# Kernel tuning notes

Measured on AMD Instinct MI355X. Metric: run time of the kernel, lower is better.

Reference implementation:

```python
import jax, jax.numpy as jnp
import numpy as np
from jax import lax

NEG_SLOPE = 0.1

def leaky(x):
    return jnp.where(x >= 0, x, NEG_SLOPE * x)

def soft_pool(x, n_p):
    # x: (B, F, P) -> (B, F, N_p, F), faithful to the torch per-channel topk+gather
    xs = jax.nn.softmax(x, axis=1)
    _, idx = lax.top_k(xs, n_p)                 # idx: (B, F, N_p), indices into P per channel
    # sp_cube[b, c, n, f] = xs[b, c, idx[b, f, n]]
    g = jnp.take_along_axis(xs[:, :, None, :], idx[:, None, :, :], axis=3)  # (B, F, F, N_p)
    return jnp.transpose(g, (0, 1, 3, 2))       # (B, F, N_p, F)

def setup_inputs() -> dict:
    key = jax.random.key(0)
    ks = jax.random.split(key, 16)
    B, C, H, W, M = 32, 5, 64, 64, 8
    s = 0.02
    inp = {
        'coor_feat': jax.random.uniform(ks[0], (B, C, H, W), jnp.float32),
        'region': jax.random.uniform(ks[1], (B, M, H, W), jnp.float32),
        'extents': jax.random.uniform(ks[2], (B, 3), jnp.float32),
        'w1': jax.random.normal(ks[3], (128, C), jnp.float32) * s,
        'b1': jnp.zeros((128,), jnp.float32),
        'w2': jax.random.normal(ks[4], (128, 128), jnp.float32) * s,
        'b2': jnp.zeros((128,), jnp.float32),
        'w3': jax.random.normal(ks[5], (128, 128), jnp.float32) * s,
        'b3': jnp.zeros((128,), jnp.float32),
        'w_sp': jax.random.normal(ks[6], (128, 128, 128), jnp.float32) * s,  # (out, in, k) for Conv2d(128,128,(1,128))
        'b_sp': jnp.zeros((128,), jnp.float32),
        'fc1_w': jax.random.normal(ks[7], (512, 128 * 8), jnp.float32) * s,
        'fc1_b': jnp.zeros((512,), jnp.float32),
        'fc2_w': jax.random.normal(ks[8], (256, 512), jnp.float32) * s,
        'fc2_b': jnp.zeros((256,), jnp.float32),
        'fcr_w': jax.random.normal(ks[9], (4, 256), jnp.float32) * 0.01,
        'fcr_b': jnp.zeros((4,), jnp.float32),
        'fct_w': jax.random.normal(ks[10], (3, 256), jnp.float32) * 0.01,
        'fct_b': jnp.zeros((3,), jnp.float32),
    }
    return inp

def reference(coor_feat, region, extents, w1, b1, w2, b2, w3, b3, w_sp, b_sp,
              fc1_w, fc1_b, fc2_w, fc2_b, fcr_w, fcr_b, fct_w, fct_b):
    bs, in_c, fh, fw = coor_feat.shape
    num_regions = region.shape[1]
    # denormalize xyz channels by extents (in_c == 5 path)
    xyz = (coor_feat[:, :3] - 0.5) * extents[:, :, None, None]
    x = jnp.concatenate([xyz, coor_feat[:, 3:]], axis=1)
    x = x.reshape(bs, in_c, fh * fw)                          # (B, C, P)
    # 1x1 Conv1d stack
    x = leaky(jnp.einsum('bip,oi->bop', x, w1) + b1[None, :, None])
    x = leaky(jnp.einsum('bip,oi->bop', x, w2) + b2[None, :, None])
    x = jnp.einsum('bip,oi->bop', x, w3) + b3[None, :, None]  # (B, 128, P)
    # region-masked multiply: (B,128,M,P)
    xm = x[:, :, None, :] * region.reshape(bs, 1, num_regions, fh * fw)
    # spatial max pool over P
    x = jnp.max(xm, axis=-1)                                  # (B, 128, M)
    # region softpool
    sp = soft_pool(x, num_regions)                            # (B, 128, M(=N_p), 128)
    x = leaky(jnp.einsum('bcrk,ock->bor', sp, w_sp) + b_sp[None, :, None])  # conv_sp
    x = x.reshape(bs, -1)                                     # (B, 1024)
    x = leaky(x @ fc1_w.T + fc1_b)
    x = leaky(x @ fc2_w.T + fc2_b)
    rot = x @ fcr_w.T + fcr_b
    t = x @ fct_w.T + fct_b
    return (rot, t)
```

## Files before the change

kernel.cpp:

```cpp
#include <hip/hip_runtime.h>
#include <cstddef>
#include <cstdint>

#define LEAKY(s) ((s) >= 0.f ? (s) : 0.1f * (s))

constexpr int PTS    = 4096;
constexpr int NBATCH = 32;
constexpr int NM     = 8;
constexpr int TILE   = 128;
constexpr int NTILES = PTS / TILE;

constexpr size_t OFF_POOL = 0;
constexpr size_t OFF_WSP  = 131072;
constexpr size_t OFF_Y32  = 262144;
constexpr size_t OFF_Y    = 4456448;
constexpr size_t OFF_H1   = 4587520;

using bf16x8 = __attribute__((ext_vector_type(8))) short;
using f32x4v = __attribute__((ext_vector_type(4))) float;
using u16x4  = __attribute__((ext_vector_type(4))) unsigned short;
using u16x8  = __attribute__((ext_vector_type(8))) unsigned short;

__device__ __forceinline__ unsigned short rbf(float x) {
  unsigned u = __float_as_uint(x);
  return (unsigned short)((u + 0x7FFFu + ((u >> 16) & 1u)) >> 16);
}

__device__ __forceinline__ unsigned encf(float f) {
  unsigned u = __float_as_uint(f);
  return (u & 0x80000000u) ? ~u : (u | 0x80000000u);
}
__device__ __forceinline__ float decf(unsigned e) {
  unsigned u = (e & 0x80000000u) ? (e ^ 0x80000000u) : ~e;
  return __uint_as_float(u);
}

__device__ __forceinline__ int swzb(int pt, int kByte) {
  return pt * 256 + (kByte ^ ((pt & 7) << 4));
}

__global__ __launch_bounds__(256) void kW(const float* __restrict__ w2,
                                          const float* __restrict__ w3,
                                          unsigned short* __restrict__ wsp,
                                          unsigned* __restrict__ pool) {
  int id = blockIdx.x * 256 + threadIdx.x;
  pool[id] = 0u;
  int layer = id >> 14, e16 = id & 16383;
  int e = e16 & 7, l15 = (e16 >> 3) & 15, l4 = (e16 >> 7) & 3,
      kt = (e16 >> 9) & 3, mt = e16 >> 11;
  int c = mt * 16 + l15, k = kt * 32 + l4 * 8 + e;
  float v = (layer ? w3 : w2)[c * 128 + k];
  wsp[layer * 16384 + e16] = rbf(v);
}

__device__ __forceinline__ void mfmaLayer8s(const unsigned short* __restrict__ W,
                                            const float* __restrict__ bias,
                                            const char* Xc,
                                            int lane, int mt, f32x4v acc[8]) {
  const int l15 = lane & 15, l4 = lane >> 4;
  {
    float4 bv = *(const float4*)(bias + mt * 16 + l4 * 4);
    f32x4v b4; b4[0] = bv.x; b4[1] = bv.y; b4[2] = bv.z; b4[3] = bv.w;
#pragma unroll
    for (int nt = 0; nt < 8; nt++) acc[nt] = b4;
  }
#pragma unroll
  for (int kt = 0; kt < 4; kt++) {
    int woff = (((mt * 4 + kt) * 4 + l4) * 16 + l15) * 8;
    bf16x8 ah = *(const bf16x8*)(W + woff);
    const int kb = (kt * 32 + l4 * 8) * 2;
#pragma unroll
    for (int nt = 0; nt < 8; nt++) {
      bf16x8 bh = *(const bf16x8*)(Xc + swzb(nt * 16 + l15, kb));
      acc[nt] = __builtin_amdgcn_mfma_f32_16x16x32_bf16(ah, bh, acc[nt], 0, 0, 0);
    }
  }
}

__global__ __launch_bounds__(512, 8) void kA(
    const float* __restrict__ coor, const float* __restrict__ region,
    const float* __restrict__ extents,
    const float* __restrict__ w1, const float* __restrict__ b1,
    const float* __restrict__ b2, const float* __restrict__ b3,
    const unsigned short* __restrict__ wsp,
    unsigned* __restrict__ pool) {
  __shared__ unsigned short X[128 * 128];
  __shared__ float reg_s[NM * TILE];
  const int tid = threadIdx.x;
  const int b = blockIdx.y;
  const int t0 = blockIdx.x * TILE;
  const int lane = tid & 63;
  const int wv = tid >> 6;
  char* Xc = (char*)X;

  {
    int m = tid >> 6, j = tid & 63;
    float2 v = *(const float2*)(region + ((size_t)b * NM + m) * PTS + t0 + j * 2);
    *(float2*)(reg_s + m * TILE + j * 2) = v;
  }
  {
    const int pt = tid & 127;
    const int chq = (tid >> 7) * 32;
    float e0 = extents[b * 3], e1 = extents[b * 3 + 1], e2 = extents[b * 3 + 2];
    float in5[5];
#pragma unroll
    for (int i = 0; i < 5; i++) in5[i] = coor[((size_t)b * 5 + i) * PTS + t0 + pt];
    in5[0] = (in5[0] - 0.5f) * e0;
    in5[1] = (in5[1] - 0.5f) * e1;
    in5[2] = (in5[2] - 0.5f) * e2;
#pragma unroll
    for (int c8 = 0; c8 < 32; c8 += 8) {
      u16x8 hh;
#pragma unroll
      for (int q = 0; q < 8; q++) {
        int c = chq + c8 + q;
        float s = b1[c];
#pragma unroll
        for (int i = 0; i < 5; i++) s = fmaf(w1[c * 5 + i], in5[i], s);
        s = LEAKY(s);
        hh[q] = rbf(s);
      }
      int off = swzb(pt, (chq + c8) * 2);
      *(u16x8*)(Xc + off) = hh;
    }
  }
  __syncthreads();

  f32x4v acc[8];
  const int mt = wv;
  const int l15 = lane & 15, l4 = lane >> 4;

  mfmaLayer8s(wsp, b2, Xc, lane, mt, acc);
  __syncthreads();
  {
    const int ch0 = mt * 16 + l4 * 4;
#pragma unroll
    for (int nt = 0; nt < 8; nt++) {
      u16x4 h4;
#pragma unroll
      for (int r = 0; r < 4; r++) {
        float s = acc[nt][r];
        s = LEAKY(s);
        h4[r] = rbf(s);
      }
      int off = swzb(nt * 16 + l15, ch0 * 2);
      *(u16x4*)(Xc + off) = h4;
    }
  }
  __syncthreads();
  mfmaLayer8s(wsp + 16384, b3, Xc, lane, mt, acc);
  __syncthreads();

  {
    float* funnel = (float*)X;
#pragma unroll
    for (int m = 0; m < NM; m++) {
      float rv[8];
#pragma unroll
      for (int nt = 0; nt < 8; nt++) rv[nt] = reg_s[m * TILE + nt * 16 + l15];
#pragma unroll
      for (int r = 0; r < 4; r++) {
        float mx = acc[0][r] * rv[0];
#pragma unroll
        for (int nt = 1; nt < 8; nt++) mx = fmaxf(mx, acc[nt][r] * rv[nt]);
        mx = fmaxf(mx, __shfl_xor(mx, 1));
        mx = fmaxf(mx, __shfl_xor(mx, 2));
        mx = fmaxf(mx, __shfl_xor(mx, 4));
        mx = fmaxf(mx, __shfl_xor(mx, 8));
        if (l15 == 0) funnel[(mt * 16 + l4 * 4 + r) * 8 + m] = mx;
      }
    }
  }
  __syncthreads();
  {
    const float* fun = (const float*)X;
    unsigned* pl = pool + (size_t)b * 1024;
    atomicMax(pl + tid, encf(fun[tid]));
    atomicMax(pl + tid + 512, encf(fun[tid + 512]));
  }
}

__global__ __launch_bounds__(256) void kC(const unsigned* __restrict__ pool,
                                          const float* __restrict__ w_sp,
                                          float* __restrict__ y32) {
  __shared__ float As[16 * 516];
  __shared__ float xsl[4 * 128 * 8];
  __shared__ int idxL[4][4][8];
  const int tid = threadIdx.x;
  const int k0 = blockIdx.x * 4;
  const int bbase = blockIdx.y * 4;
  const int rg = tid & 63, cgq = tid >> 6;

#pragma unroll
  for (int it = 0; it < 4; it++) {
    uint4 v = *(const uint4*)(pool + (size_t)(bbase + it) * 1024 + tid * 4);
    float4 f = {decf(v.x), decf(v.y), decf(v.z), decf(v.w)};
    *(float4*)(xsl + it * 1024 + tid * 4) = f;
  }
  float4 wreg[8];
#pragma unroll
  for (int it = 0; it < 8; it++) {
    int q = tid + it * 256, o = q >> 4, cc = q & 15;
    wreg[it] = *(const float4*)(w_sp + (size_t)o * 16384 + (size_t)cc * 128 + k0);
  }
  __syncthreads();
  {
    int pair = tid >> 3, sub = tid & 7;
    int bl = pair >> 3, m = pair & 7;
    float* base = xsl + bl * 1024 + m;
    float v[16];
#pragma unroll
    for (int j = 0; j < 16; j++) v[j] = base[(sub + 8 * j) * 8];
    float mx = v[0];
#pragma unroll
    for (int j = 1; j < 16; j++) mx = fmaxf(mx, v[j]);
    mx = fmaxf(mx, __shfl_xor(mx, 1));
    mx = fmaxf(mx, __shfl_xor(mx, 2));
    mx = fmaxf(mx, __shfl_xor(mx, 4));
    float s = 0.f;
#pragma unroll
    for (int j = 0; j < 16; j++) { v[j] = expf(v[j] - mx); s += v[j]; }
    s += __shfl_xor(s, 1);
    s += __shfl_xor(s, 2);
    s += __shfl_xor(s, 4);
    float inv = 1.f / s;
#pragma unroll
    for (int j = 0; j < 16; j++) base[(sub + 8 * j) * 8] = v[j] * inv;
  }
  __syncthreads();
  if (tid < 16) {
    int bl = tid >> 2, kk = tid & 3;
    float vv[8];
#pragma unroll
    for (int n = 0; n < 8; n++) vv[n] = xsl[bl * 1024 + (k0 + kk) * 8 + n];
    int used = 0;
#pragma unroll
    for (int n = 0; n < 8; n++) {
      int best = 0; float bv = -1.f;
#pragma unroll
      for (int q = 0; q < 8; q++) {
        bool ok = ((used >> q) & 1) == 0;
        if (ok && vv[q] > bv) { bv = vv[q]; best = q; }
      }
      used |= 1 << best;
      idxL[bl][kk][n] = best;
    }
  }

  float acc[8][8];
#pragma unroll
  for (int i = 0; i < 8; i++)
#pragma unroll
    for (int j = 0; j < 8; j++) acc[i][j] = 0.f;

  for (int c0 = 0; c0 < 128; c0 += 16) {
    __syncthreads();
#pragma unroll
    for (int it = 0; it < 8; it++) {
      int q = tid + it * 256, o = q >> 4, cc = q & 15;
      As[cc * 516 + o]       = wreg[it].x;
      As[cc * 516 + 128 + o] = wreg[it].y;
      As[cc * 516 + 256 + o] = wreg[it].z;
      As[cc * 516 + 384 + o] = wreg[it].w;
    }
    __syncthreads();
    if (c0 + 16 < 128) {
#pragma unroll
      for (int it = 0; it < 8; it++) {
        int q = tid + it * 256, o = q >> 4, cc = q & 15;
        wreg[it] = *(const float4*)(w_sp + (size_t)o * 16384 + (size_t)(c0 + 16 + cc) * 128 + k0);
      }
    }
#pragma unroll
    for (int cc = 0; cc < 16; cc++) {
      float4 a0 = *(const float4*)(As + cc * 516 + rg * 4);
      float4 a1 = *(const float4*)(As + cc * 516 + 256 + rg * 4);
      float4 p0 = *(const float4*)(xsl + cgq * 1024 + (c0 + cc) * 8);
      float4 p1 = *(const float4*)(xsl + cgq * 1024 + (c0 + cc) * 8 + 4);
      float av[8] = {a0.x, a0.y, a0.z, a0.w, a1.x, a1.y, a1.z, a1.w};
      float bv[8] = {p0.x, p0.y, p0.z, p0.w, p1.x, p1.y, p1.z, p1.w};
#pragma unroll
      for (int i = 0; i < 8; i++)
#pragma unroll
        for (int j = 0; j < 8; j++) acc[i][j] = fmaf(av[i], bv[j], acc[i][j]);
    }
  }
  const int rgl = rg & 31;
  const int kkA = rg >> 5;
  int msA[8], msB[8];
#pragma unroll
  for (int r = 0; r < 8; r++) {
    msA[r] = idxL[cgq][kkA][r];
    msB[r] = idxL[cgq][2 + kkA][r];
  }
  float yp[4][8];
#pragma unroll
  for (int i4 = 0; i4 < 4; i4++) {
#pragma unroll
    for (int r = 0; r < 8; r++) {
      float v = 0.f;
#pragma unroll
      for (int j = 0; j < 8; j++) {
        v += (j == msA[r]) ? acc[i4][j] : 0.f;
        v += (j == msB[r]) ? acc[i4 + 4][j] : 0.f;
      }
      yp[i4][r] = v;
    }
  }
#pragma unroll
  for (int i4 = 0; i4 < 4; i4++)
#pragma unroll
    for (int r = 0; r < 8; r++) yp[i4][r] += __shfl_xor(yp[i4][r], 32);
  if (rg < 32) {
    float* dst = y32 + ((size_t)(bbase + cgq) * 32 + blockIdx.x) * 1024 + rgl * 32;
#pragma unroll
    for (int i4 = 0; i4 < 4; i4++) {
      float4 v0 = {yp[i4][0], yp[i4][1], yp[i4][2], yp[i4][3]};
      float4 v1 = {yp[i4][4], yp[i4][5], yp[i4][6], yp[i4][7]};
      *(float4*)(dst + i4 * 8) = v0;
      *(float4*)(dst + i4 * 8 + 4) = v1;
    }
  }
}

__global__ __launch_bounds__(256) void kY(const float* __restrict__ y32,
                                          const float* __restrict__ b_sp,
                                          float* __restrict__ y) {
  int fg = blockIdx.x, b = blockIdx.y, tid = threadIdx.x;
  int f = fg * 256 + tid;
  const float* base = y32 + (size_t)b * 32768 + f;
  float s = 0.f;
#pragma unroll 8
  for (int t = 0; t < 32; t++) s += base[t * 1024];
  s += b_sp[f >> 3];
  y[(size_t)b * 1024 + f] = LEAKY(s);
}

__global__ __launch_bounds__(256) void kE1(
    const float* __restrict__ y, const float* __restrict__ fc1_w,
    const float* __restrict__ fc1_b, float* __restrict__ h1) {
  int og = blockIdx.x, b = blockIdx.y, tid = threadIdx.x;
  int wid = tid >> 6, lane = tid & 63;
  const float4* yv = (const float4*)(y + (size_t)b * 1024);
  float4 u[4];
#pragma unroll
  for (int r = 0; r < 4; r++) u[r] = yv[r * 64 + lane];
#pragma unroll 4
  for (int pass = 0; pass < 16; pass++) {
    int o = og * 64 + pass * 4 + wid;
    const float4* wr = (const float4*)(fc1_w + (size_t)o * 1024);
    float sa = 0, sb = 0, sc = 0, sd = 0;
#pragma unroll
    for (int r = 0; r < 4; r++) {
      float4 wv = wr[r * 64 + lane];
      sa = fmaf(wv.x, u[r].x, sa); sb = fmaf(wv.y, u[r].y, sb);
      sc = fmaf(wv.z, u[r].z, sc); sd = fmaf(wv.w, u[r].w, sd);
    }
    float s = (sa + sb) + (sc + sd);
#pragma unroll
    for (int d = 1; d < 64; d <<= 1) s += __shfl_xor(s, d);
    if (lane == 0) {
      float t = s + fc1_b[o];
      h1[(size_t)b * 512 + o] = LEAKY(t);
    }
  }
}

__global__ __launch_bounds__(1024) void kE2(
    const float* __restrict__ h1, const float* __restrict__ fc2_w,
    const float* __restrict__ fc2_b,
    const float* __restrict__ fcr_w, const float* __restrict__ fcr_b,
    const float* __restrict__ fct_w, const float* __restrict__ fct_b,
    float* __restrict__ out) {
  __shared__ float h1l[512];
  __shared__ float h2[256];
  int b = blockIdx.x, tid = threadIdx.x;
  int w = tid >> 6, lane = tid & 63;
  if (tid < 128) {
    float4 v = ((const float4*)(h1 + (size_t)b * 512))[tid];
    ((float4*)h1l)[tid] = v;
  }
  __syncthreads();
  {
    const float4* h1v = (const float4*)h1l;
    float4 u0 = h1v[lane], u1 = h1v[64 + lane];
#pragma unroll 2
    for (int pass = 0; pass < 16; pass++) {
      int o = w * 16 + pass;
      const float4* wr = (const float4*)(fc2_w + (size_t)o * 512);
      float4 w0 = wr[lane], w1 = wr[64 + lane];
      float sa = fmaf(w0.x, u0.x, 0.f), sb = fmaf(w0.y, u0.y, 0.f);
      float sc = fmaf(w0.z, u0.z, 0.f), sd = fmaf(w0.w, u0.w, 0.f);
      sa = fmaf(w1.x, u1.x, sa); sb = fmaf(w1.y, u1.y, sb);
      sc = fmaf(w1.z, u1.z, sc); sd = fmaf(w1.w, u1.w, sd);
      float s = (sa + sb) + (sc + sd);
#pragma unroll
      for (int d = 1; d < 64; d <<= 1) s += __shfl_xor(s, d);
      if (lane == 0) {
        float t = s + fc2_b[o];
        h2[o] = LEAKY(t);
      }
    }
  }
  __syncthreads();
  if (w < 7) {
    bool isrot = w < 4;
    int o = isrot ? w : w - 4;
    const float4* wr = (const float4*)((isrot ? fcr_w : fct_w) + (size_t)o * 256);
    const float4* uv = (const float4*)h2;
    float4 wv = wr[lane];
    float4 u = uv[lane];
    float s = fmaf(wv.x, u.x, fmaf(wv.y, u.y, fmaf(wv.z, u.z, wv.w * u.w)));
#pragma unroll
    for (int d = 1; d < 64; d <<= 1) s += __shfl_xor(s, d);
    if (lane == 0) {
      float t = s + (isrot ? fcr_b[o] : fct_b[o]);
      out[isrot ? (b * 4 + o) : (128 + b * 3 + o)] = t;
    }
  }
}

extern "C" void kernel_launch(void* const* d_in, const int* in_sizes, int n_in,
                              void* d_out, int out_size, void* d_ws, size_t ws_size,
                              hipStream_t stream) {
  const float* coor    = (const float*)d_in[0];
  const float* region  = (const float*)d_in[1];
  const float* extents = (const float*)d_in[2];
  const float* w1 = (const float*)d_in[3];  const float* b1 = (const float*)d_in[4];
  const float* w2 = (const float*)d_in[5];  const float* b2 = (const float*)d_in[6];
  const float* w3 = (const float*)d_in[7];  const float* b3 = (const float*)d_in[8];
  const float* w_sp = (const float*)d_in[9];  const float* b_sp = (const float*)d_in[10];
  const float* fc1_w = (const float*)d_in[11]; const float* fc1_b = (const float*)d_in[12];
  const float* fc2_w = (const float*)d_in[13]; const float* fc2_b = (const float*)d_in[14];
  const float* fcr_w = (const float*)d_in[15]; const float* fcr_b = (const float*)d_in[16];
  const float* fct_w = (const float*)d_in[17]; const float* fct_b = (const float*)d_in[18];

  char* ws = (char*)d_ws;
  unsigned* pool = (unsigned*)(ws + OFF_POOL);
  unsigned short* wsp = (unsigned short*)(ws + OFF_WSP);
  float* y32  = (float*)(ws + OFF_Y32);
  float* y    = (float*)(ws + OFF_Y);
  float* h1   = (float*)(ws + OFF_H1);
  float* out  = (float*)d_out;

  kW<<<dim3(128), 256, 0, stream>>>(w2, w3, wsp, pool);
  kA<<<dim3(NTILES, NBATCH), 512, 0, stream>>>(coor, region, extents,
                                               w1, b1, b2, b3, wsp, pool);
  kC<<<dim3(32, 8), 256, 0, stream>>>(pool, w_sp, y32);
  kY<<<dim3(4, NBATCH), 256, 0, stream>>>(y32, b_sp, y);
  kE1<<<dim3(8, NBATCH), 256, 0, stream>>>(y, fc1_w, fc1_b, h1);
  kE2<<<dim3(NBATCH), 1024, 0, stream>>>(h1, fc2_w, fc2_b, fcr_w, fcr_b,
                                         fct_w, fct_b, out);
}
```

Before: 108.4 us.

## Split softmax/top-k into separate kernel and retile conv_sp over output channels

Moves the per-batch softmax and top-k index selection out of kC into a new kB kernel that writes softmax values and indices to workspace. The old kC recomputed these for every k-tile block. kC is now tiled by k and output-channel groups with all 32 batches per block, so each block loads its w_sp slice once instead of re-streaming the whole weight per batch group. The gather is done through shared memory in four passes. This adds one kernel launch and extra workspace traffic, and raises shared-memory use.

Result: slower. 131.1 us (+20.9%).

```diff
diff --git a/kernel.cpp b/kernel.cpp
--- a/kernel.cpp
+++ b/kernel.cpp
@@ -12,9 +12,11 @@
 
 constexpr size_t OFF_POOL = 0;
 constexpr size_t OFF_WSP  = 131072;
-constexpr size_t OFF_Y32  = 262144;
-constexpr size_t OFF_Y    = 4456448;
-constexpr size_t OFF_H1   = 4587520;
+constexpr size_t OFF_XS   = 196608;
+constexpr size_t OFF_IDX  = 327680;
+constexpr size_t OFF_Y32  = 458752;
+constexpr size_t OFF_Y    = 4653056;
+constexpr size_t OFF_H1   = 4784128;
 
 using bf16x8 = __attribute__((ext_vector_type(8))) short;
 using f32x4v = __attribute__((ext_vector_type(4))) float;
@@ -180,71 +182,97 @@
   }
 }
 
-__global__ __launch_bounds__(256) void kC(const unsigned* __restrict__ pool,
+__global__ __launch_bounds__(256) void kB(const unsigned* __restrict__ pool,
+                                          float* __restrict__ xs,
+                                          int* __restrict__ idx) {
+  __shared__ float pl[1024];
+  __shared__ float xsl[1024];
+  int b = blockIdx.x, tid = threadIdx.x;
+#pragma unroll
+  for (int q = 0; q < 4; q++) {
+    int p = tid + q * 256;
+    pl[p] = decf(pool[(size_t)b * 1024 + p]);
+  }
+  __syncthreads();
+  int m = tid >> 5, lane = tid & 31;
+  float v[4];
+#pragma unroll
+  for (int j = 0; j < 4; j++) v[j] = pl[(lane + 32 * j) * 8 + m];
+  float mx = fmaxf(fmaxf(v[0], v[1]), fmaxf(v[2], v[3]));
+#pragma unroll
+  for (int d = 1; d < 32; d <<= 1) mx = fmaxf(mx, __shfl_xor(mx, d, 32));
+  float e[4]; float s = 0.f;
+#pragma unroll
+  for (int j = 0; j < 4; j++) { e[j] = expf(v[j] - mx); s += e[j]; }
+#pragma unroll
+  for (int d = 1; d < 32; d <<= 1) s += __shfl_xor(s, d, 32);
+#pragma unroll
+  for (int j = 0; j < 4; j++) {
+    float x = e[j] / s;
+    int c = lane + 32 * j;
+    xsl[c * 8 + m] = x;
+    xs[(size_t)b * 1024 + c * 8 + m] = x;
+  }
+  __syncthreads();
+  if (tid < 128) {
+    float vv[8];
+#pragma unroll
+    for (int n = 0; n < 8; n++) vv[n] = xsl[tid * 8 + n];
+    int used = 0;
+#pragma unroll
+    for (int n = 0; n < 8; n++) {
+      int best = 0; float bvv = -1.f;
+#pragma unroll
+      for (int q = 0; q < 8; q++) {
+        bool ok = ((used >> q) & 1) == 0;
+        if (ok && vv[q] > bvv) { bvv = vv[q]; best = q; }
+      }
+      used |= 1 << best;
+      idx[(size_t)b * 1024 + tid * 8 + n] = best;
+    }
+  }
+}
+
+__global__ __launch_bounds__(256) void kC(const float* __restrict__ xs,
+                                          const int* __restrict__ idx,
                                           const float* __restrict__ w_sp,
                                           float* __restrict__ y32) {
-  __shared__ float As[16 * 516];
-  __shared__ float xsl[4 * 128 * 8];
-  __shared__ int idxL[4][4][8];
+  __shared__ float Ws[128 * 68];
+  __shared__ float Bs[16 * 256];
+  __shared__ int idxL[32][4][8];
   const int tid = threadIdx.x;
-  const int k0 = blockIdx.x * 4;
-  const int bbase = blockIdx.y * 4;
-  const int rg = tid & 63, cgq = tid >> 6;
-
+  const int kt = blockIdx.x, og = blockIdx.y;
+  const int k0 = kt * 4, o0 = og * 16;
+  const int rowq = tid >> 5;
+  const int bcol = tid & 31;
+  const int kown = rowq >> 1;
+
+#pragma unroll
+  for (int it = 0; it < 8; it++) {
+    int f = it * 256 + tid;
+    int o15 = f >> 7, c = f & 127;
+    float4 w = *(const float4*)(w_sp + (size_t)(o0 + o15) * 16384 + (size_t)c * 128 + k0);
+    float* wc = Ws + c * 68;
+    wc[o15]      = w.x;
+    wc[16 + o15] = w.y;
+    wc[32 + o15] = w.z;
+    wc[48 + o15] = w.w;
+  }
+  {
+    int g0 = tid * 4;
+#pragma unroll
+    for (int j = 0; j < 4; j++) {
+      int g = g0 + j;
+      int b = g >> 5, kk = (g >> 3) & 3, r = g & 7;
+      idxL[b][kk][r] = idx[(size_t)b * 1024 + (k0 + kk) * 8 + r];
+    }
+  }
+  float4 breg[4];
 #pragma unroll
   for (int it = 0; it < 4; it++) {
-    uint4 v = *(const uint4*)(pool + (size_t)(bbase + it) * 1024 + tid * 4);
-    float4 f = {decf(v.x), decf(v.y), decf(v.z), decf(v.w)};
-    *(float4*)(xsl + it * 1024 + tid * 4) = f;
-  }
-  float4 wreg[8];
-#pragma unroll
-  for (int it = 0; it < 8; it++) {
-    int q = tid + it * 256, o = q >> 4, cc = q & 15;
-    wreg[it] = *(const float4*)(w_sp + (size_t)o * 16384 + (size_t)cc * 128 + k0);
-  }
-  __syncthreads();
-  {
-    int pair = tid >> 3, sub = tid & 7;
-    int bl = pair >> 3, m = pair & 7;
-    float* base = xsl + bl * 1024 + m;
-    float v[16];
-#pragma unroll
-    for (int j = 0; j < 16; j++) v[j] = base[(sub + 8 * j) * 8];
-    float mx = v[0];
-#pragma unroll
-    for (int j = 1; j < 16; j++) mx = fmaxf(mx, v[j]);
-    mx = fmaxf(mx, __shfl_xor(mx, 1));
-    mx = fmaxf(mx, __shfl_xor(mx, 2));
-    mx = fmaxf(mx, __shfl_xor(mx, 4));
-    float s = 0.f;
-#pragma unroll
-    for (int j = 0; j < 16; j++) { v[j] = expf(v[j] - mx); s += v[j]; }
-    s += __shfl_xor(s, 1);
-    s += __shfl_xor(s, 2);
-    s += __shfl_xor(s, 4);
-    float inv = 1.f / s;
-#pragma unroll
-    for (int j = 0; j < 16; j++) base[(sub + 8 * j) * 8] = v[j] * inv;
-  }
-  __syncthreads();
-  if (tid < 16) {
-    int bl = tid >> 2, kk = tid & 3;
-    float vv[8];
-#pragma unroll
-    for (int n = 0; n < 8; n++) vv[n] = xsl[bl * 1024 + (k0 + kk) * 8 + n];
-    int used = 0;
-#pragma unroll
-    for (int n = 0; n < 8; n++) {
-      int best = 0; float bv = -1.f;
-#pragma unroll
-      for (int q = 0; q < 8; q++) {
-        bool ok = ((used >> q) & 1) == 0;
-        if (ok && vv[q] > bv) { bv = vv[q]; best = q; }
-      }
-      used |= 1 << best;
-      idxL[bl][kk][n] = best;
-    }
+    int f = it * 256 + tid;
+    int b = f & 31, mq = (f >> 5) & 1, cc = f >> 6;
+    breg[it] = *(const float4*)(xs + (size_t)b * 1024 + (size_t)cc * 8 + mq * 4);
   }
 
   float acc[8][8];
@@ -256,71 +284,63 @@
   for (int c0 = 0; c0 < 128; c0 += 16) {
     __syncthreads();
 #pragma unroll
-    for (int it = 0; it < 8; it++) {
-      int q = tid + it * 256, o = q >> 4, cc = q & 15;
-      As[cc * 516 + o]       = wreg[it].x;
-      As[cc * 516 + 128 + o] = wreg[it].y;
-      As[cc * 516 + 256 + o] = wreg[it].z;
-      As[cc * 516 + 384 + o] = wreg[it].w;
+    for (int it = 0; it < 4; it++) {
+      int f = it * 256 + tid;
+      int b = f & 31, mq = (f >> 5) & 1, cc = f >> 6;
+      *(float4*)(Bs + cc * 256 + mq * 128 + b * 4) = breg[it];
     }
     __syncthreads();
     if (c0 + 16 < 128) {
 #pragma unroll
-      for (int it = 0; it < 8; it++) {
-        int q = tid + it * 256, o = q >> 4, cc = q & 15;
-        wreg[it] = *(const float4*)(w_sp + (size_t)o * 16384 + (size_t)(c0 + 16 + cc) * 128 + k0);
+      for (int it = 0; it < 4; it++) {
+        int f = it * 256 + tid;
+        int b = f & 31, mq = (f >> 5) & 1, cc = f >> 6;
+        breg[it] = *(const float4*)(xs + (size_t)b * 1024 + (size_t)(c0 + 16 + cc) * 8 + mq * 4);
       }
     }
 #pragma unroll
     for (int cc = 0; cc < 16; cc++) {
-      float4 a0 = *(const float4*)(As + cc * 516 + rg * 4);
-      float4 a1 = *(const float4*)(As + cc * 516 + 256 + rg * 4);
-      float4 p0 = *(const float4*)(xsl + cgq * 1024 + (c0 + cc) * 8);
-      float4 p1 = *(const float4*)(xsl + cgq * 1024 + (c0 + cc) * 8 + 4);
-      float av[8] = {a0.x, a0.y, a0.z, a0.w, a1.x, a1.y, a1.z, a1.w};
-      float bv[8] = {p0.x, p0.y, p0.z, p0.w, p1.x, p1.y, p1.z, p1.w};
+      const float* wc = Ws + (c0 + cc) * 68 + rowq * 8;
+      float4 w0 = *(const float4*)(wc);
+      float4 w1 = *(const float4*)(wc + 4);
+      float4 b0 = *(const float4*)(Bs + cc * 256 + bcol * 4);
+      float4 b1 = *(const float4*)(Bs + cc * 256 + 128 + bcol * 4);
+      float av[8] = {w0.x, w0.y, w0.z, w0.w, w1.x, w1.y, w1.z, w1.w};
+      float bv[8] = {b0.x, b0.y, b0.z, b0.w, b1.x, b1.y, b1.z, b1.w};
 #pragma unroll
       for (int i = 0; i < 8; i++)
 #pragma unroll
         for (int j = 0; j < 8; j++) acc[i][j] = fmaf(av[i], bv[j], acc[i][j]);
     }
   }
-  const int rgl = rg & 31;
-  const int kkA = rg >> 5;
-  int msA[8], msB[8];
-#pragma unroll
-  for (int r = 0; r < 8; r++) {
-    msA[r] = idxL[cgq][kkA][r];
-    msB[r] = idxL[cgq][2 + kkA][r];
-  }
-  float yp[4][8];
-#pragma unroll
-  for (int i4 = 0; i4 < 4; i4++) {
-#pragma unroll
-    for (int r = 0; r < 8; r++) {
-      float v = 0.f;
-#pragma unroll
-      for (int j = 0; j < 8; j++) {
-        v += (j == msA[r]) ? acc[i4][j] : 0.f;
-        v += (j == msB[r]) ? acc[i4 + 4][j] : 0.f;
-      }
-      yp[i4][r] = v;
-    }
-  }
-#pragma unroll
-  for (int i4 = 0; i4 < 4; i4++)
-#pragma unroll
-    for (int r = 0; r < 8; r++) yp[i4][r] += __shfl_xor(yp[i4][r], 32);
-  if (rg < 32) {
-    float* dst = y32 + ((size_t)(bbase + cgq) * 32 + blockIdx.x) * 1024 + rgl * 32;
-#pragma unroll
-    for (int i4 = 0; i4 < 4; i4++) {
-      float4 v0 = {yp[i4][0], yp[i4][1], yp[i4][2], yp[i4][3]};
-      float4 v1 = {yp[i4][4], yp[i4][5], yp[i4][6], yp[i4][7]};
-      *(float4*)(dst + i4 * 8) = v0;
-      *(float4*)(dst + i4 * 8 + 4) = v1;
-    }
-  }
+  float* Dsh = Bs;
+  float yacc[16];
+#pragma unroll
+  for (int o = 0; o < 16; o++) yacc[o] = 0.f;
+  const int bown = tid >> 3, rown = tid & 7;
+#pragma unroll
+  for (int pass = 0; pass < 4; pass++) {
+    __syncthreads();
+    if (kown == pass) {
+#pragma unroll
+      for (int i = 0; i < 8; i++) {
+        int op = (rowq & 1) * 8 + i;
+        float* dp = Dsh + op * 256 + bcol * 4;
+        float4 v0 = {acc[i][0], acc[i][1], acc[i][2], acc[i][3]};
+        float4 v1 = {acc[i][4], acc[i][5], acc[i][6], acc[i][7]};
+        *(float4*)(dp) = v0;
+        *(float4*)(dp + 128) = v1;
+      }
+    }
+    __syncthreads();
+    int m = idxL[bown][pass][rown];
+    int moff = (m >> 2) * 128 + (m & 3);
+#pragma unroll
+    for (int o = 0; o < 16; o++) yacc[o] += Dsh[o * 256 + moff + bown * 4];
+  }
+  float* dst = y32 + (size_t)bown * 32768 + (size_t)kt * 1024 + (size_t)o0 * 8 + rown;
+#pragma unroll
+  for (int o = 0; o < 16; o++) dst[o * 8] = yacc[o];
 }
 
 __global__ __launch_bounds__(256) void kY(const float* __restrict__ y32,
@@ -438,6 +458,8 @@
   char* ws = (char*)d_ws;
   unsigned* pool = (unsigned*)(ws + OFF_POOL);
   unsigned short* wsp = (unsigned short*)(ws + OFF_WSP);
+  float* xs   = (float*)(ws + OFF_XS);
+  int*   idx  = (int*)(ws + OFF_IDX);
   float* y32  = (float*)(ws + OFF_Y32);
   float* y    = (float*)(ws + OFF_Y);
   float* h1   = (float*)(ws + OFF_H1);
@@ -446,7 +468,8 @@
   kW<<<dim3(128), 256, 0, stream>>>(w2, w3, wsp, pool);
   kA<<<dim3(NTILES, NBATCH), 512, 0, stream>>>(coor, region, extents,
                                                w1, b1, b2, b3, wsp, pool);
-  kC<<<dim3(32, 8), 256, 0, stream>>>(pool, w_sp, y32);
+  kB<<<dim3(NBATCH), 256, 0, stream>>>(pool, xs, idx);
+  kC<<<dim3(32, 8), 256, 0, stream>>>(xs, idx, w_sp, y32);
   kY<<<dim3(4, NBATCH), 256, 0, stream>>>(y32, b_sp, y);
   kE1<<<dim3(8, NBATCH), 256, 0, stream>>>(y, fc1_w, fc1_b, h1);
   kE2<<<dim3(NBATCH), 1024, 0, stream>>>(h1, fc2_w, fc2_b, fcr_w, fcr_b,
```

## Run first conv layer on MFMA and split kC over output-channel halves

Applied to the files above, without the earlier changes.

The first 5-to-128 pointwise layer moves from per-thread scalar FMAs to a single bf16 MFMA per tile, using a zero-padded 32-wide K layout that kW prepares for w1 and stages in a small shared buffer. The kA occupancy hint drops from 8 to 6 waves. kC now splits output channels into two halves over a 1D grid of 512 blocks with remapped indices, halving per-block registers and shared memory so more blocks run in parallel. This removes the scalar layer-1 work and kC's low parallelism, at the cost of rounding the layer-1 inputs to bf16 and an extra shuffle reduction.

New measurement: 93.26 us (median of 2 runs). -14.0%, faster.

```diff
diff --git a/kernel.cpp b/kernel.cpp
--- a/kernel.cpp
+++ b/kernel.cpp
@@ -39,18 +39,26 @@
   return pt * 256 + (kByte ^ ((pt & 7) << 4));
 }
 
-__global__ __launch_bounds__(256) void kW(const float* __restrict__ w2,
+__global__ __launch_bounds__(256) void kW(const float* __restrict__ w1,
+                                          const float* __restrict__ w2,
                                           const float* __restrict__ w3,
                                           unsigned short* __restrict__ wsp,
                                           unsigned* __restrict__ pool) {
   int id = blockIdx.x * 256 + threadIdx.x;
   pool[id] = 0u;
-  int layer = id >> 14, e16 = id & 16383;
-  int e = e16 & 7, l15 = (e16 >> 3) & 15, l4 = (e16 >> 7) & 3,
-      kt = (e16 >> 9) & 3, mt = e16 >> 11;
-  int c = mt * 16 + l15, k = kt * 32 + l4 * 8 + e;
-  float v = (layer ? w3 : w2)[c * 128 + k];
-  wsp[layer * 16384 + e16] = rbf(v);
+  {
+    int layer = id >> 14, e16 = id & 16383;
+    int e = e16 & 7, l15 = (e16 >> 3) & 15, l4 = (e16 >> 7) & 3,
+        kt = (e16 >> 9) & 3, mt = e16 >> 11;
+    int c = mt * 16 + l15, k = kt * 32 + l4 * 8 + e;
+    float v = (layer ? w3 : w2)[c * 128 + k];
+    wsp[4096 + layer * 16384 + e16] = rbf(v);
+  }
+  if (id < 4096) {
+    int e = id & 7, l15 = (id >> 3) & 15, l4 = (id >> 7) & 3, mt = id >> 9;
+    int c = mt * 16 + l15, k = l4 * 8 + e;
+    wsp[id] = (k < 5) ? rbf(w1[c * 5 + k]) : (unsigned short)0;
+  }
 }
 
 __device__ __forceinline__ void mfmaLayer8s(const unsigned short* __restrict__ W,
@@ -77,14 +85,15 @@
   }
 }
 
-__global__ __launch_bounds__(512, 8) void kA(
+__global__ __launch_bounds__(512, 6) void kA(
     const float* __restrict__ coor, const float* __restrict__ region,
     const float* __restrict__ extents,
-    const float* __restrict__ w1, const float* __restrict__ b1,
-    const float* __restrict__ b2, const float* __restrict__ b3,
+    const float* __restrict__ b1, const float* __restrict__ b2,
+    const float* __restrict__ b3,
     const unsigned short* __restrict__ wsp,
     unsigned* __restrict__ pool) {
   __shared__ unsigned short X[128 * 128];
+  __shared__ unsigned short X5[128 * 40];
   __shared__ float reg_s[NM * TILE];
   const int tid = threadIdx.x;
   const int b = blockIdx.y;
@@ -92,6 +101,7 @@
   const int lane = tid & 63;
   const int wv = tid >> 6;
   char* Xc = (char*)X;
+  char* X5c = (char*)X5;
 
   {
     int m = tid >> 6, j = tid & 63;
@@ -100,29 +110,20 @@
   }
   {
     const int pt = tid & 127;
-    const int chq = (tid >> 7) * 32;
-    float e0 = extents[b * 3], e1 = extents[b * 3 + 1], e2 = extents[b * 3 + 2];
-    float in5[5];
-#pragma unroll
-    for (int i = 0; i < 5; i++) in5[i] = coor[((size_t)b * 5 + i) * PTS + t0 + pt];
-    in5[0] = (in5[0] - 0.5f) * e0;
-    in5[1] = (in5[1] - 0.5f) * e1;
-    in5[2] = (in5[2] - 0.5f) * e2;
-#pragma unroll
-    for (int c8 = 0; c8 < 32; c8 += 8) {
-      u16x8 hh;
-#pragma unroll
-      for (int q = 0; q < 8; q++) {
-        int c = chq + c8 + q;
-        float s = b1[c];
-#pragma unroll
-        for (int i = 0; i < 5; i++) s = fmaf(w1[c * 5 + i], in5[i], s);
-        s = LEAKY(s);
-        hh[q] = rbf(s);
-      }
-      int off = swzb(pt, (chq + c8) * 2);
-      *(u16x8*)(Xc + off) = hh;
-    }
+    const int part = tid >> 7;
+    u16x8 hh = {0, 0, 0, 0, 0, 0, 0, 0};
+    if (part == 0) {
+      float e0 = extents[b * 3], e1 = extents[b * 3 + 1], e2 = extents[b * 3 + 2];
+      float in5[5];
+#pragma unroll
+      for (int i = 0; i < 5; i++) in5[i] = coor[((size_t)b * 5 + i) * PTS + t0 + pt];
+      in5[0] = (in5[0] - 0.5f) * e0;
+      in5[1] = (in5[1] - 0.5f) * e1;
+      in5[2] = (in5[2] - 0.5f) * e2;
+#pragma unroll
+      for (int q = 0; q < 5; q++) hh[q] = rbf(in5[q]);
+    }
+    *(u16x8*)(X5c + pt * 80 + part * 16) = hh;
   }
   __syncthreads();
 
@@ -130,8 +131,18 @@
   const int mt = wv;
   const int l15 = lane & 15, l4 = lane >> 4;
 
-  mfmaLayer8s(wsp, b2, Xc, lane, mt, acc);
-  __syncthreads();
+  {
+    float4 bv = *(const float4*)(b1 + mt * 16 + l4 * 4);
+    f32x4v b4; b4[0] = bv.x; b4[1] = bv.y; b4[2] = bv.z; b4[3] = bv.w;
+#pragma unroll
+    for (int nt = 0; nt < 8; nt++) acc[nt] = b4;
+    bf16x8 ah = *(const bf16x8*)(wsp + ((mt * 4 + l4) * 16 + l15) * 8);
+#pragma unroll
+    for (int nt = 0; nt < 8; nt++) {
+      bf16x8 bh = *(const bf16x8*)(X5c + (nt * 16 + l15) * 80 + l4 * 16);
+      acc[nt] = __builtin_amdgcn_mfma_f32_16x16x32_bf16(ah, bh, acc[nt], 0, 0, 0);
+    }
+  }
   {
     const int ch0 = mt * 16 + l4 * 4;
 #pragma unroll
@@ -148,7 +159,26 @@
     }
   }
   __syncthreads();
-  mfmaLayer8s(wsp + 16384, b3, Xc, lane, mt, acc);
+
+  mfmaLayer8s(wsp + 4096, b2, Xc, lane, mt, acc);
+  __syncthreads();
+  {
+    const int ch0 = mt * 16 + l4 * 4;
+#pragma unroll
+    for (int nt = 0; nt < 8; nt++) {
+      u16x4 h4;
+#pragma unroll
+      for (int r = 0; r < 4; r++) {
+        float s = acc[nt][r];
+        s = LEAKY(s);
+        h4[r] = rbf(s);
+      }
+      int off = swzb(nt * 16 + l15, ch0 * 2);
+      *(u16x4*)(Xc + off) = h4;
+    }
+  }
+  __syncthreads();
+  mfmaLayer8s(wsp + 20480, b3, Xc, lane, mt, acc);
   __syncthreads();
 
   {
@@ -183,12 +213,17 @@
 __global__ __launch_bounds__(256) void kC(const unsigned* __restrict__ pool,
                                           const float* __restrict__ w_sp,
                                           float* __restrict__ y32) {
-  __shared__ float As[16 * 516];
+  __shared__ float As[16 * 260];
   __shared__ float xsl[4 * 128 * 8];
   __shared__ int idxL[4][4][8];
   const int tid = threadIdx.x;
-  const int k0 = blockIdx.x * 4;
-  const int bbase = blockIdx.y * 4;
+  const int id = blockIdx.x;
+  const int kt = (id & 7) | ((id >> 7) << 3);
+  const int bg = (id >> 3) & 7;
+  const int og2 = (id >> 6) & 1;
+  const int k0 = kt * 4;
+  const int o0 = og2 * 64;
+  const int bbase = bg * 4;
   const int rg = tid & 63, cgq = tid >> 6;
 
 #pragma unroll
@@ -197,11 +232,11 @@
     float4 f = {decf(v.x), decf(v.y), decf(v.z), decf(v.w)};
     *(float4*)(xsl + it * 1024 + tid * 4) = f;
   }
-  float4 wreg[8];
-#pragma unroll
-  for (int it = 0; it < 8; it++) {
+  float4 wreg[4];
+#pragma unroll
+  for (int it = 0; it < 4; it++) {
     int q = tid + it * 256, o = q >> 4, cc = q & 15;
-    wreg[it] = *(const float4*)(w_sp + (size_t)o * 16384 + (size_t)cc * 128 + k0);
+    wreg[it] = *(const float4*)(w_sp + (size_t)(o0 + o) * 16384 + (size_t)cc * 128 + k0);
   }
   __syncthreads();
   {
@@ -247,52 +282,47 @@
     }
   }
 
-  float acc[8][8];
-#pragma unroll
-  for (int i = 0; i < 8; i++)
+  float acc[4][8];
+#pragma unroll
+  for (int i = 0; i < 4; i++)
 #pragma unroll
     for (int j = 0; j < 8; j++) acc[i][j] = 0.f;
 
   for (int c0 = 0; c0 < 128; c0 += 16) {
     __syncthreads();
 #pragma unroll
-    for (int it = 0; it < 8; it++) {
+    for (int it = 0; it < 4; it++) {
       int q = tid + it * 256, o = q >> 4, cc = q & 15;
-      As[cc * 516 + o]       = wreg[it].x;
-      As[cc * 516 + 128 + o] = wreg[it].y;
-      As[cc * 516 + 256 + o] = wreg[it].z;
-      As[cc * 516 + 384 + o] = wreg[it].w;
+      As[cc * 260 + o]       = wreg[it].x;
+      As[cc * 260 + 64 + o]  = wreg[it].y;
+      As[cc * 260 + 128 + o] = wreg[it].z;
+      As[cc * 260 + 192 + o] = wreg[it].w;
     }
     __syncthreads();
     if (c0 + 16 < 128) {
 #pragma unroll
-      for (int it = 0; it < 8; it++) {
+      for (int it = 0; it < 4; it++) {
         int q = tid + it * 256, o = q >> 4, cc = q & 15;
-        wreg[it] = *(const float4*)(w_sp + (size_t)o * 16384 + (size_t)(c0 + 16 + cc) * 128 + k0);
+        wreg[it] = *(const float4*)(w_sp + (size_t)(o0 + o) * 16384 + (size_t)(c0 + 16 + cc) * 128 + k0);
       }
     }
 #pragma unroll
     for (int cc = 0; cc < 16; cc++) {
-      float4 a0 = *(const float4*)(As + cc * 516 + rg * 4);
-      float4 a1 = *(const float4*)(As + cc * 516 + 256 + rg * 4);
+      float4 a = *(const float4*)(As + cc * 260 + rg * 4);
       float4 p0 = *(const float4*)(xsl + cgq * 1024 + (c0 + cc) * 8);
       float4 p1 = *(const float4*)(xsl + cgq * 1024 + (c0 + cc) * 8 + 4);
-      float av[8] = {a0.x, a0.y, a0.z, a0.w, a1.x, a1.y, a1.z, a1.w};
+      float av[4] = {a.x, a.y, a.z, a.w};
       float bv[8] = {p0.x, p0.y, p0.z, p0.w, p1.x, p1.y, p1.z, p1.w};
 #pragma unroll
-      for (int i = 0; i < 8; i++)
+      for (int i = 0; i < 4; i++)
 #pragma unroll
         for (int j = 0; j < 8; j++) acc[i][j] = fmaf(av[i], bv[j], acc[i][j]);
     }
   }
-  const int rgl = rg & 31;
-  const int kkA = rg >> 5;
-  int msA[8], msB[8];
-#pragma unroll
-  for (int r = 0; r < 8; r++) {
-    msA[r] = idxL[cgq][kkA][r];
-    msB[r] = idxL[cgq][2 + kkA][r];
-  }
+  const int kk = rg >> 4;
+  int ms[8];
+#pragma unroll
+  for (int r = 0; r < 8; r++) ms[r] = idxL[cgq][kk][r];
   float yp[4][8];
 #pragma unroll
   for (int i4 = 0; i4 < 4; i4++) {
@@ -300,19 +330,19 @@
     for (int r = 0; r < 8; r++) {
       float v = 0.f;
 #pragma unroll
-      for (int j = 0; j < 8; j++) {
-        v += (j == msA[r]) ? acc[i4][j] : 0.f;
-        v += (j == msB[r]) ? acc[i4 + 4][j] : 0.f;
-      }
+      for (int j = 0; j < 8; j++) v += (j == ms[r]) ? acc[i4][j] : 0.f;
       yp[i4][r] = v;
     }
   }
 #pragma unroll
   for (int i4 = 0; i4 < 4; i4++)
 #pragma unroll
-    for (int r = 0; r < 8; r++) yp[i4][r] += __shfl_xor(yp[i4][r], 32);
-  if (rg < 32) {
-    float* dst = y32 + ((size_t)(bbase + cgq) * 32 + blockIdx.x) * 1024 + rgl * 32;
+    for (int r = 0; r < 8; r++) {
+      yp[i4][r] += __shfl_xor(yp[i4][r], 16);
+      yp[i4][r] += __shfl_xor(yp[i4][r], 32);
+    }
+  if (rg < 16) {
+    float* dst = y32 + ((size_t)(bbase + cgq) * 32 + kt) * 1024 + (size_t)(o0 + rg * 4) * 8;
 #pragma unroll
     for (int i4 = 0; i4 < 4; i4++) {
       float4 v0 = {yp[i4][0], yp[i4][1], yp[i4][2], yp[i4][3]};
@@ -443,10 +473,10 @@
   float* h1   = (float*)(ws + OFF_H1);
   float* out  = (float*)d_out;
 
-  kW<<<dim3(128), 256, 0, stream>>>(w2, w3, wsp, pool);
+  kW<<<dim3(128), 256, 0, stream>>>(w1, w2, w3, wsp, pool);
   kA<<<dim3(NTILES, NBATCH), 512, 0, stream>>>(coor, region, extents,
-                                               w1, b1, b2, b3, wsp, pool);
-  kC<<<dim3(32, 8), 256, 0, stream>>>(pool, w_sp, y32);
+                                               b1, b2, b3, wsp, pool);
+  kC<<<dim3(512), 256, 0, stream>>>(pool, w_sp, y32);
   kY<<<dim3(4, NBATCH), 256, 0, stream>>>(y32, b_sp, y);
   kE1<<<dim3(8, NBATCH), 256, 0, stream>>>(y, fc1_w, fc1_b, h1);
   kE2<<<dim3(NBATCH), 1024, 0, stream>>>(h1, fc2_w, fc2_b, fcr_w, fcr_b,
```
